# Kernel tuning notes

Measured on AMD Instinct MI355X. Metric: run time of the kernel, lower is better.

Reference implementation:

```python
import jax, jax.numpy as jnp
import numpy as np

B, N, M, K = 128, 128, 16, 8      # graphs, nodes/graph, num_samples, pearl_k
H_MLP = 16                        # pearl_mlp_out
D_PE = 64                         # pe_dims (GIN hidden/out)
E = 262144
BN_EPS = 1e-5


def setup_inputs() -> dict:
    key = jax.random.key(0)
    ks = jax.random.split(key, 16)
    lap = jax.random.normal(ks[0], (B, N, N), dtype=jnp.float32) * 0.1
    W0 = jax.random.normal(ks[1], (B, N, M), dtype=jnp.float32)
    edge_index = jax.random.randint(ks[2], (2, E), 0, B * N, dtype=jnp.int32)
    s = lambda k, sh, fan: jax.random.normal(k, sh, dtype=jnp.float32) / np.sqrt(fan)
    return {
        "lap": lap,
        "W0": W0,
        "mlp_W": s(ks[3], (K, H_MLP), K),
        "mlp_b": jnp.zeros((H_MLP,), jnp.float32),
        "bn_g": jnp.ones((H_MLP,), jnp.float32),
        "bn_b": jnp.zeros((H_MLP,), jnp.float32),
        "eps1": jnp.zeros((), jnp.float32),
        "W1a": s(ks[4], (H_MLP, D_PE), H_MLP),
        "b1a": jnp.zeros((D_PE,), jnp.float32),
        "W1b": s(ks[5], (D_PE, D_PE), D_PE),
        "b1b": jnp.zeros((D_PE,), jnp.float32),
        "eps2": jnp.zeros((), jnp.float32),
        "W2a": s(ks[6], (D_PE, D_PE), D_PE),
        "b2a": jnp.zeros((D_PE,), jnp.float32),
        "W2b": s(ks[7], (D_PE, D_PE), D_PE),
        "b2b": jnp.zeros((D_PE,), jnp.float32),
        "edge_index": edge_index,
    }


def _gin_layer(h, eps, Wa, ba, Wb, bb, src, dst, num_nodes):
    # h: [Nsum, M, D]; GIN aggregation: (1+eps)*h + sum_{j in N(i)} h_j
    agg = jax.ops.segment_sum(h[src], dst, num_segments=num_nodes)
    z = (1.0 + eps) * h + agg
    z = jax.nn.relu(jnp.einsum("nmd,de->nme", z, Wa) + ba)
    z = jnp.einsum("nmd,de->nme", z, Wb) + bb
    return jax.nn.relu(z)


def reference(lap, W0, mlp_W, mlp_b, bn_g, bn_b, eps1, W1a, b1a, W1b, b1b,
              eps2, W2a, b2a, W2b, b2b, edge_index):
    # polynomial filter: stack [W, S@W, S^2@W, ...]  -> [B, N, M, K]
    out = W0
    ws = [out]
    for _ in range(K - 1):
        out = jnp.einsum("bij,bjm->bim", lap, out)
        ws.append(out)
    feat = jnp.stack(ws, axis=-1)                       # [B, N, M, K]

    # per-graph MLP over trailing k dim + BatchNorm1d (training stats, per graph)
    h = jnp.einsum("bnmk,kh->bnmh", feat, mlp_W) + mlp_b  # [B, N, M, H]
    mu = jnp.mean(h, axis=(1, 2), keepdims=True)
    var = jnp.var(h, axis=(1, 2), keepdims=True)
    h = (h - mu) * jax.lax.rsqrt(var + BN_EPS) * bn_g + bn_b
    h = jax.nn.relu(h)

    # concat graphs -> [Nsum, M, H]; GIN over batched edge_index
    h = h.reshape(B * N, M, H_MLP)
    src, dst = edge_index[0], edge_index[1]
    h = _gin_layer(h, eps1, W1a, b1a, W1b, b1b, src, dst, B * N)
    h = _gin_layer(h, eps2, W2a, b2a, W2b, b2b, src, dst, B * N)

    # RandomSampleAggregator: sum over the sample dim -> [Nsum, D_pe]
    return h.sum(axis=1)
```

## Files before the change

### kernel.cpp

```cpp
#include <hip/hip_runtime.h>

typedef unsigned short u16;
typedef unsigned int   u32;
typedef short bf16x8 __attribute__((ext_vector_type(8)));
typedef float f32x4  __attribute__((ext_vector_type(4)));
typedef float f32x2  __attribute__((ext_vector_type(2)));

#define BG    128
#define NN    128
#define MS    16
#define KP    8
#define HM    16
#define DP    64
#define NSUM  16384
#define NE    262144
#define SITES 2048


__device__ __forceinline__ float blo(u32 u){ union{u32 i; float f;} v; v.i=u<<16; return v.f; }
__device__ __forceinline__ float bhi(u32 u){ union{u32 i; float f;} v; v.i=u&0xffff0000u; return v.f; }
__device__ __forceinline__ u16  f2b(float f){ union{float f; u32 i;} v; v.f=f; u32 x=v.i; x += 0x7fffu + ((x>>16)&1u); return (u16)(x>>16); }
__device__ __forceinline__ u32  pk2(float a, float b){ return (u32)f2b(a) | ((u32)f2b(b)<<16); }
__device__ __forceinline__ f32x2 up2(u32 u){ f32x2 v; v.x=blo(u); v.y=bhi(u); return v; }

__device__ __forceinline__ void fsplit(float x, short& hi, short& lo){
  u16 h = f2b(x); hi = (short)h; lo = (short)f2b(x - blo((u32)h));
}

#define MFMA16(a,b,c) __builtin_amdgcn_mfma_f32_16x16x32_bf16(a,b,c,0,0,0)

__device__ __forceinline__ bf16x8 bfragW(const float* __restrict__ W, int nrows,
                                         int k0, int nb, int col, int quad){
  bf16x8 f;
  #pragma unroll
  for(int j=0;j<8;++j){
    int k = k0 + quad*8 + j;
    float v = (k < nrows) ? W[k*DP + nb + col] : 0.f;
    f[j] = (short)f2b(v);
  }
  return f;
}
__device__ __forceinline__ bf16x8 afragT(const float* tp){
  float4 v0 = *(const float4*)tp;
  float4 v1 = *(const float4*)(tp+4);
  bf16x8 a;
  a[0]=(short)f2b(v0.x); a[1]=(short)f2b(v0.y); a[2]=(short)f2b(v0.z); a[3]=(short)f2b(v0.w);
  a[4]=(short)f2b(v1.x); a[5]=(short)f2b(v1.y); a[6]=(short)f2b(v1.z); a[7]=(short)f2b(v1.w);
  return a;
}

__global__ __launch_bounds__(256,1) void k_poly(
    const float* __restrict__ lap, const float* __restrict__ W0, const float* __restrict__ mlpW,
    const float* __restrict__ bng, const float* __restrict__ bnb, u16* __restrict__ h1T,
    int* __restrict__ cnt)
{
  __shared__ float Wbuf[2][SITES];
  __shared__ float mlpWS[KP*HM];
  __shared__ float red[4][32];
  __shared__ float stat[32];
  __shared__ float ssc[HM], ssh[HM];

  const int b = blockIdx.x, t = threadIdx.x, l = t&63, w = t>>6;
  const int col = l&15, quad = l>>4;
  if (t < 128) cnt[b*128 + t] = 0;

  {
    const float4* src = (const float4*)(W0 + (size_t)b*SITES);
    for (int i=t; i<SITES/4; i+=256) ((float4*)Wbuf[0])[i] = src[i];
    if (t < KP*HM) mlpWS[t] = mlpW[t];
  }

  bf16x8 Ah[2][4], Al[2][4];
  {
    const float* lg = lap + (size_t)b*NN*NN;
    #pragma unroll
    for(int Mt=0;Mt<2;++Mt){
      const int nr = w*32 + Mt*16 + col;
      #pragma unroll
      for(int Kc=0;Kc<4;++Kc){
        const float* p = lg + (size_t)nr*NN + Kc*32 + quad*8;
        float4 v0 = *(const float4*)p;
        float4 v1 = *(const float4*)(p+4);
        float xs[8] = {v0.x,v0.y,v0.z,v0.w,v1.x,v1.y,v1.z,v1.w};
        #pragma unroll
        for(int j=0;j<8;++j){ short hi,lo; fsplit(xs[j],hi,lo); Ah[Mt][Kc][j]=hi; Al[Mt][Kc][j]=lo; }
      }
    }
  }

  float h[8][16];
  {
    const float* w0g = W0 + (size_t)b*SITES;
    #pragma unroll
    for(int Mt=0;Mt<2;++Mt){
      #pragma unroll
      for(int r=0;r<4;++r){
        const int n = w*32 + Mt*16 + quad*4 + r;
        float sv = w0g[n*MS + col];
        #pragma unroll
        for(int c=0;c<16;++c) h[Mt*4+r][c] = sv*mlpW[c];
      }
    }
  }
  __syncthreads();

  int cur=0;
  for(int k=1;k<KP;++k){
    f32x4 c0 = {0.f,0.f,0.f,0.f};
    f32x4 c1 = {0.f,0.f,0.f,0.f};
    #pragma unroll
    for(int Kc=0;Kc<4;++Kc){
      const float* wb = &Wbuf[cur][(Kc*32 + quad*8)*MS + col];
      bf16x8 Bh, Bl;
      #pragma unroll
      for(int j=0;j<8;++j){
        float x = wb[j*MS];
        short hi,lo; fsplit(x,hi,lo); Bh[j]=hi; Bl[j]=lo;
      }
      c0 = MFMA16(Ah[0][Kc], Bh, c0);
      c0 = MFMA16(Ah[0][Kc], Bl, c0);
      c0 = MFMA16(Al[0][Kc], Bh, c0);
      c1 = MFMA16(Ah[1][Kc], Bh, c1);
      c1 = MFMA16(Ah[1][Kc], Bl, c1);
      c1 = MFMA16(Al[1][Kc], Bh, c1);
    }
    float mw[16];
    #pragma unroll
    for(int c=0;c<16;++c) mw[c]=mlpWS[k*16+c];
    #pragma unroll
    for(int r=0;r<4;++r){
      const int n0 = w*32 + quad*4 + r;
      Wbuf[cur^1][n0*MS + col]        = c0[r];
      Wbuf[cur^1][(n0+16)*MS + col]   = c1[r];
      #pragma unroll
      for(int c=0;c<16;++c){ h[r][c] += c0[r]*mw[c]; h[4+r][c] += c1[r]*mw[c]; }
    }
    __syncthreads();
    cur ^= 1;
  }

  float sum[16], sq[16];
  #pragma unroll
  for(int c=0;c<16;++c){ sum[c]=0.f; sq[c]=0.f; }
  #pragma unroll
  for(int s=0;s<8;++s){
    #pragma unroll
    for(int c=0;c<16;++c){ float v=h[s][c]; sum[c]+=v; sq[c]+=v*v; }
  }
  #pragma unroll
  for(int d=1;d<64;d<<=1){
    #pragma unroll
    for(int c=0;c<16;++c){ sum[c]+=__shfl_xor(sum[c],d,64); sq[c]+=__shfl_xor(sq[c],d,64); }
  }
  if(l==0){
    #pragma unroll
    for(int c=0;c<16;++c){ red[w][c]=sum[c]; red[w][16+c]=sq[c]; }
  }
  __syncthreads();
  if(t<32) stat[t]=red[0][t]+red[1][t]+red[2][t]+red[3][t];
  __syncthreads();
  if(t<16){
    float mu  = stat[t]*(1.f/SITES);
    float var = stat[16+t]*(1.f/SITES) - mu*mu;
    float sc  = bng[t] * rsqrtf(var + 1e-5f);
    ssc[t]=sc; ssh[t]=bnb[t] - mu*sc;
  }
  __syncthreads();
  {
    float sc[16], sh[16];
    #pragma unroll
    for(int c=0;c<16;++c){ sc[c]=ssc[c]; sh[c]=ssh[c]; }
    #pragma unroll
    for(int s=0;s<8;++s){
      const int n = w*32 + (s>>2)*16 + quad*4 + (s&3);
      const int node = b*NN + n;
      float r[16];
      #pragma unroll
      for(int c=0;c<16;++c) r[c]=fmaxf(h[s][c]*sc[c]+sh[c], 0.f);
      uint4 A;
      A.x=pk2(r[0],r[1]);  A.y=pk2(r[2],r[3]);  A.z=pk2(r[4],r[5]);  A.w=pk2(r[6],r[7]);
      uint4 Bv;
      Bv.x=pk2(r[8],r[9]); Bv.y=pk2(r[10],r[11]); Bv.z=pk2(r[12],r[13]); Bv.w=pk2(r[14],r[15]);
      u16* o = h1T + ((size_t)col*NSUM + node)*HM;
      *(uint4*)o     = A;
      *(uint4*)(o+8) = Bv;
    }
  }
}

__global__ void k_hist(const int* __restrict__ dst, int* __restrict__ cnt){
  int e = blockIdx.x*256 + threadIdx.x;
  atomicAdd(&cnt[dst[e]], 1);
}

__global__ void k_scan(const int* __restrict__ cnt, int* __restrict__ off, int* __restrict__ wpos){
  __shared__ int ps[256];
  const int t = threadIdx.x, PER = NSUM/256;
  int s=0;
  for(int i=0;i<PER;++i) s += cnt[t*PER+i];
  ps[t]=s; __syncthreads();
  for(int d=1; d<256; d<<=1){
    int v = (t>=d) ? ps[t-d] : 0;
    __syncthreads();
    ps[t] += v;
    __syncthreads();
  }
  int run = (t==0) ? 0 : ps[t-1];
  for(int i=0;i<PER;++i){
    int idx=t*PER+i;
    off[idx]=run; wpos[idx]=run;
    run += cnt[idx];
  }
  if(t==255) off[NSUM]=run;
}

__global__ void k_scatter(const int* __restrict__ srcI, const int* __restrict__ dstI,
                          int* __restrict__ wpos, int* __restrict__ srcs){
  int e = blockIdx.x*256 + threadIdx.x;
  int p = atomicAdd(&wpos[dstI[e]], 1);
  srcs[p] = srcI[e];
}

__global__ __launch_bounds__(256) void k_agg1(
  const u16* __restrict__ h1T, const float* __restrict__ eps1p,
  const int* __restrict__ off, const int* __restrict__ srcs, u16* __restrict__ z1)
{
  const int t=threadIdx.x, l=t&63, w=t>>6;
  const int m = blockIdx.x & 15, g = blockIdx.x >> 4;
  const int grp = l>>2, q = l&3;
  const int node = g*64 + w*16 + grp;
  const float epe = 1.f + eps1p[0];
  const u16* __restrict__ base = h1T + (size_t)m*NSUM*HM;

  f32x2 A[2];
  {
    uint2 x = *(const uint2*)&base[(size_t)node*HM + q*4];
    f32x2 s2; s2.x=epe; s2.y=epe;
    A[0]=s2*up2(x.x); A[1]=s2*up2(x.y);
  }
  const int e0 = off[node], e1 = off[node+1];
  int dmax = e1 - e0;
  #pragma unroll
  for(int d=1; d<64; d<<=1) dmax = max(dmax, __shfl_xor(dmax, d, 64));

  int i = 0;
  for(; i+2 <= dmax; i += 2){
    int pa = e0+i, pb = e0+i+1;
    float sa = (pa < e1) ? 1.f : 0.f;
    float sb = (pb < e1) ? 1.f : 0.f;
    int ea = min(pa, NE-1), eb = min(pb, NE-1);
    int ia = srcs[ea], ib = srcs[eb];
    uint2 xa = *(const uint2*)&base[(size_t)ia*HM + q*4];
    uint2 xb = *(const uint2*)&base[(size_t)ib*HM + q*4];
    f32x2 va; va.x=sa; va.y=sa;
    f32x2 vb; vb.x=sb; vb.y=sb;
    A[0]+=va*up2(xa.x); A[1]+=va*up2(xa.y);
    A[0]+=vb*up2(xb.x); A[1]+=vb*up2(xb.y);
  }
  if(i < dmax){
    int pa = e0+i;
    float sa = (pa < e1) ? 1.f : 0.f;
    int ea = min(pa, NE-1);
    int ia = srcs[ea];
    uint2 xa = *(const uint2*)&base[(size_t)ia*HM + q*4];
    f32x2 va; va.x=sa; va.y=sa;
    A[0]+=va*up2(xa.x); A[1]+=va*up2(xa.y);
  }

  uint2 o; o.x=pk2(A[0].x,A[0].y); o.y=pk2(A[1].x,A[1].y);
  *(uint2*)&z1[(size_t)node*256 + m*HM + q*4] = o;
}

__global__ __launch_bounds__(256) void k_agg2(
  const u16* __restrict__ h2T, const float* __restrict__ eps2p,
  const int* __restrict__ off, const int* __restrict__ srcs, u16* __restrict__ z2)
{
  const int t=threadIdx.x, l=t&63, w=t>>6;
  const int m = blockIdx.x & 15, g = blockIdx.x >> 4;
  const int grp = l>>3, q = l&7;
  const int node = g*32 + w*8 + grp;
  const float epe = 1.f + eps2p[0];
  const u16* __restrict__ base = h2T + (size_t)m*NSUM*DP;

  f32x2 A[4];
  {
    uint4 x = *(const uint4*)&base[(size_t)node*DP + q*8];
    f32x2 s2; s2.x=epe; s2.y=epe;
    A[0]=s2*up2(x.x); A[1]=s2*up2(x.y); A[2]=s2*up2(x.z); A[3]=s2*up2(x.w);
  }
  const int e0 = off[node], e1 = off[node+1];
  int dmax = e1 - e0;
  #pragma unroll
  for(int d=1; d<64; d<<=1) dmax = max(dmax, __shfl_xor(dmax, d, 64));

  int i = 0;
  for(; i+2 <= dmax; i += 2){
    int pa = e0+i, pb = e0+i+1;
    float sa = (pa < e1) ? 1.f : 0.f;
    float sb = (pb < e1) ? 1.f : 0.f;
    int ea = min(pa, NE-1), eb = min(pb, NE-1);
    int ia = srcs[ea], ib = srcs[eb];
    uint4 xa = *(const uint4*)&base[(size_t)ia*DP + q*8];
    uint4 xb = *(const uint4*)&base[(size_t)ib*DP + q*8];
    f32x2 va; va.x=sa; va.y=sa;
    f32x2 vb; vb.x=sb; vb.y=sb;
    A[0]+=va*up2(xa.x); A[1]+=va*up2(xa.y); A[2]+=va*up2(xa.z); A[3]+=va*up2(xa.w);
    A[0]+=vb*up2(xb.x); A[1]+=vb*up2(xb.y); A[2]+=vb*up2(xb.z); A[3]+=vb*up2(xb.w);
  }
  if(i < dmax){
    int pa = e0+i;
    float sa = (pa < e1) ? 1.f : 0.f;
    int ea = min(pa, NE-1);
    int ia = srcs[ea];
    uint4 xa = *(const uint4*)&base[(size_t)ia*DP + q*8];
    f32x2 va; va.x=sa; va.y=sa;
    A[0]+=va*up2(xa.x); A[1]+=va*up2(xa.y); A[2]+=va*up2(xa.z); A[3]+=va*up2(xa.w);
  }

  uint4 o;
  o.x=pk2(A[0].x,A[0].y); o.y=pk2(A[1].x,A[1].y);
  o.z=pk2(A[2].x,A[2].y); o.w=pk2(A[3].x,A[3].y);
  *(uint4*)&z2[(size_t)node*1024 + m*DP + q*8] = o;
}

__global__ __launch_bounds__(256) void k_mm1(
  const u16* __restrict__ z1, const float* __restrict__ W1a, const float* __restrict__ b1a,
  const float* __restrict__ W1b, const float* __restrict__ b1b, u16* __restrict__ h2T)
{
  __shared__ float tS[4][16*68 + 4];
  const int t=threadIdx.x, l=t&63, w=t>>6;
  const int col=l&15, quad=l>>4;

  bf16x8 fa[4], fb[4][2];
  float bav[4], bbv[4];
  #pragma unroll
  for(int nt=0;nt<4;++nt){
    fa[nt]    = bfragW(W1a, HM, 0,  nt*16, col, quad);
    fb[nt][0] = bfragW(W1b, DP, 0,  nt*16, col, quad);
    fb[nt][1] = bfragW(W1b, DP, 32, nt*16, col, quad);
    bav[nt] = b1a[nt*16+col];
    bbv[nt] = b1b[nt*16+col];
  }
  for(int ni=0;ni<2;++ni){
    const int node = blockIdx.x*8 + ni*4 + w;
    bf16x8 a0;
    #pragma unroll
    for(int j=0;j<8;++j) a0[j]=0;
    if (quad < 2) a0 = *(const bf16x8*)&z1[(size_t)node*256 + col*16 + quad*8];
    #pragma unroll
    for(int nt=0;nt<4;++nt){
      f32x4 c = {bav[nt], bav[nt], bav[nt], bav[nt]};
      c = MFMA16(a0, fa[nt], c);
      #pragma unroll
      for(int r=0;r<4;++r)
        tS[w][(quad*4+r)*68 + nt*16 + col] = fmaxf(c[r], 0.f);
    }
    bf16x8 ta0 = afragT(&tS[w][col*68 + quad*8]);
    bf16x8 ta1 = afragT(&tS[w][col*68 + 32 + quad*8]);
    #pragma unroll
    for(int nt=0;nt<4;++nt){
      f32x4 c = {bbv[nt], bbv[nt], bbv[nt], bbv[nt]};
      c = MFMA16(ta0, fb[nt][0], c);
      c = MFMA16(ta1, fb[nt][1], c);
      #pragma unroll
      for(int r=0;r<4;++r)
        h2T[((size_t)(quad*4+r)*NSUM + node)*DP + nt*16 + col] = f2b(fmaxf(c[r], 0.f));
    }
  }
}

__global__ __launch_bounds__(256) void k_mm2(
  const u16* __restrict__ z2, const float* __restrict__ W2a, const float* __restrict__ b2a,
  const float* __restrict__ W2b, const float* __restrict__ b2b, float* __restrict__ out)
{
  __shared__ float tS[4][16*68 + 4];
  const int t=threadIdx.x, l=t&63, w=t>>6;
  const int col=l&15, quad=l>>4;

  bf16x8 fa[4][2], fb[4][2];
  float bav[4], bbv[4];
  #pragma unroll
  for(int nt=0;nt<4;++nt){
    fa[nt][0] = bfragW(W2a, DP, 0,  nt*16, col, quad);
    fa[nt][1] = bfragW(W2a, DP, 32, nt*16, col, quad);
    fb[nt][0] = bfragW(W2b, DP, 0,  nt*16, col, quad);
    fb[nt][1] = bfragW(W2b, DP, 32, nt*16, col, quad);
    bav[nt] = b2a[nt*16+col];
    bbv[nt] = b2b[nt*16+col];
  }
  for(int ni=0;ni<2;++ni){
    const int node = blockIdx.x*8 + ni*4 + w;
    const u16* zrow = &z2[(size_t)node*1024];
    bf16x8 a0 = *(const bf16x8*)&zrow[col*64 + quad*8];
    bf16x8 a1 = *(const bf16x8*)&zrow[col*64 + quad*8 + 32];
    #pragma unroll
    for(int nt=0;nt<4;++nt){
      f32x4 c = {bav[nt], bav[nt], bav[nt], bav[nt]};
      c = MFMA16(a0, fa[nt][0], c);
      c = MFMA16(a1, fa[nt][1], c);
      #pragma unroll
      for(int r=0;r<4;++r)
        tS[w][(quad*4+r)*68 + nt*16 + col] = fmaxf(c[r], 0.f);
    }
    bf16x8 ta0 = afragT(&tS[w][col*68 + quad*8]);
    bf16x8 ta1 = afragT(&tS[w][col*68 + 32 + quad*8]);
    #pragma unroll
    for(int nt=0;nt<4;++nt){
      f32x4 c = {bbv[nt], bbv[nt], bbv[nt], bbv[nt]};
      c = MFMA16(ta0, fb[nt][0], c);
      c = MFMA16(ta1, fb[nt][1], c);
      float s = fmaxf(c[0],0.f)+fmaxf(c[1],0.f)+fmaxf(c[2],0.f)+fmaxf(c[3],0.f);
      s += __shfl_xor(s, 16, 64);
      s += __shfl_xor(s, 32, 64);
      if (quad == 0)
        out[(size_t)node*64 + nt*16 + col] = s;
    }
  }
}

extern "C" void kernel_launch(void* const* d_in, const int* in_sizes, int n_in,
                              void* d_out, int out_size, void* d_ws, size_t ws_size,
                              hipStream_t stream)
{
  (void)in_sizes; (void)n_in; (void)out_size; (void)ws_size;
  const float* lap  = (const float*)d_in[0];
  const float* W0   = (const float*)d_in[1];
  const float* mlpW = (const float*)d_in[2];
  const float* bng  = (const float*)d_in[4];
  const float* bnb  = (const float*)d_in[5];
  const float* eps1 = (const float*)d_in[6];
  const float* W1a  = (const float*)d_in[7];
  const float* b1a  = (const float*)d_in[8];
  const float* W1b  = (const float*)d_in[9];
  const float* b1b  = (const float*)d_in[10];
  const float* eps2 = (const float*)d_in[11];
  const float* W2a  = (const float*)d_in[12];
  const float* b2a  = (const float*)d_in[13];
  const float* W2b  = (const float*)d_in[14];
  const float* b2b  = (const float*)d_in[15];
  const int*   ei   = (const int*)d_in[16];
  const int* srcI = ei;
  const int* dstI = ei + NE;

  char* ws = (char*)d_ws;
  u16* h1T  = (u16*)(ws);
  u16* z1   = (u16*)(ws + 8388608);
  u16* h2T  = (u16*)(ws + 16777216);
  u16* z2   = (u16*)(ws + 50331648);
  int* cnt  = (int*)(ws + 83886080);
  int* offA = (int*)(ws + 83951616);
  int* wpos = (int*)(ws + 84017408);
  int* srcs = (int*)(ws + 84082944);

  k_poly   <<<BG,      256, 0, stream>>>(lap, W0, mlpW, bng, bnb, h1T, cnt);
  k_hist   <<<NE/256,  256, 0, stream>>>(dstI, cnt);
  k_scan   <<<1,       256, 0, stream>>>(cnt, offA, wpos);
  k_scatter<<<NE/256,  256, 0, stream>>>(srcI, dstI, wpos, srcs);
  k_agg1   <<<16*(NSUM/64), 256, 0, stream>>>(h1T, eps1, offA, srcs, z1);
  k_mm1    <<<NSUM/8,  256, 0, stream>>>(z1, W1a, b1a, W1b, b1b, h2T);
  k_agg2   <<<16*(NSUM/32), 256, 0, stream>>>(h2T, eps2, offA, srcs, z2);
  k_mm2    <<<NSUM/8,  256, 0, stream>>>(z2, W2a, b2a, W2b, b2b, (float*)d_out);
}
```

Before: 274.7 us.

## Sort nodes by in-degree to balance wave work in GIN aggregation

Adds a single-block counting sort that orders nodes by in-degree into a permutation array (reusing the wpos buffer). Both aggregation kernels now take node indices from this permutation, so each wavefront handles nodes of similar degree and wastes fewer iterations when looping up to the wave-wide maximum degree. k_agg1 also widens each lane to 8 features (uint4 loads/stores) with 2 lanes per node, doubling nodes per wave. The cost is an extra serial single-block kernel launch and scattered output writes.

```diff
diff --git a/kernel.cpp b/kernel.cpp
--- a/kernel.cpp
+++ b/kernel.cpp
@@ -221,22 +221,50 @@
   srcs[p] = srcI[e];
 }
 
+__global__ __launch_bounds__(256) void k_sort(const int* __restrict__ cnt, int* __restrict__ perm){
+  __shared__ int bins[256];
+  __shared__ int base[256];
+  const int t = threadIdx.x;
+  bins[t]=0;
+  __syncthreads();
+  for(int i=t;i<NSUM;i+=256){
+    int d = min(cnt[i],255);
+    atomicAdd(&bins[d],1);
+  }
+  __syncthreads();
+  int v = bins[t];
+  for(int d=1; d<256; d<<=1){
+    int u = (t>=d) ? bins[t-d] : 0;
+    __syncthreads();
+    bins[t] += u;
+    __syncthreads();
+  }
+  base[t] = bins[t] - v;
+  __syncthreads();
+  for(int i=t;i<NSUM;i+=256){
+    int d = min(cnt[i],255);
+    int p = atomicAdd(&base[d],1);
+    perm[p] = i;
+  }
+}
+
 __global__ __launch_bounds__(256) void k_agg1(
   const u16* __restrict__ h1T, const float* __restrict__ eps1p,
-  const int* __restrict__ off, const int* __restrict__ srcs, u16* __restrict__ z1)
+  const int* __restrict__ off, const int* __restrict__ srcs,
+  const int* __restrict__ perm, u16* __restrict__ z1)
 {
   const int t=threadIdx.x, l=t&63, w=t>>6;
   const int m = blockIdx.x & 15, g = blockIdx.x >> 4;
-  const int grp = l>>2, q = l&3;
-  const int node = g*64 + w*16 + grp;
+  const int grp = l>>1, q = l&1;
+  const int node = perm[g*128 + w*32 + grp];
   const float epe = 1.f + eps1p[0];
   const u16* __restrict__ base = h1T + (size_t)m*NSUM*HM;
 
-  f32x2 A[2];
-  {
-    uint2 x = *(const uint2*)&base[(size_t)node*HM + q*4];
+  f32x2 A[4];
+  {
+    uint4 x = *(const uint4*)&base[(size_t)node*HM + q*8];
     f32x2 s2; s2.x=epe; s2.y=epe;
-    A[0]=s2*up2(x.x); A[1]=s2*up2(x.y);
+    A[0]=s2*up2(x.x); A[1]=s2*up2(x.y); A[2]=s2*up2(x.z); A[3]=s2*up2(x.w);
   }
   const int e0 = off[node], e1 = off[node+1];
   int dmax = e1 - e0;
@@ -250,35 +278,38 @@
     float sb = (pb < e1) ? 1.f : 0.f;
     int ea = min(pa, NE-1), eb = min(pb, NE-1);
     int ia = srcs[ea], ib = srcs[eb];
-    uint2 xa = *(const uint2*)&base[(size_t)ia*HM + q*4];
-    uint2 xb = *(const uint2*)&base[(size_t)ib*HM + q*4];
+    uint4 xa = *(const uint4*)&base[(size_t)ia*HM + q*8];
+    uint4 xb = *(const uint4*)&base[(size_t)ib*HM + q*8];
     f32x2 va; va.x=sa; va.y=sa;
     f32x2 vb; vb.x=sb; vb.y=sb;
-    A[0]+=va*up2(xa.x); A[1]+=va*up2(xa.y);
-    A[0]+=vb*up2(xb.x); A[1]+=vb*up2(xb.y);
+    A[0]+=va*up2(xa.x); A[1]+=va*up2(xa.y); A[2]+=va*up2(xa.z); A[3]+=va*up2(xa.w);
+    A[0]+=vb*up2(xb.x); A[1]+=vb*up2(xb.y); A[2]+=vb*up2(xb.z); A[3]+=vb*up2(xb.w);
   }
   if(i < dmax){
     int pa = e0+i;
     float sa = (pa < e1) ? 1.f : 0.f;
     int ea = min(pa, NE-1);
     int ia = srcs[ea];
-    uint2 xa = *(const uint2*)&base[(size_t)ia*HM + q*4];
+    uint4 xa = *(const uint4*)&base[(size_t)ia*HM + q*8];
     f32x2 va; va.x=sa; va.y=sa;
-    A[0]+=va*up2(xa.x); A[1]+=va*up2(xa.y);
-  }
-
-  uint2 o; o.x=pk2(A[0].x,A[0].y); o.y=pk2(A[1].x,A[1].y);
-  *(uint2*)&z1[(size_t)node*256 + m*HM + q*4] = o;
+    A[0]+=va*up2(xa.x); A[1]+=va*up2(xa.y); A[2]+=va*up2(xa.z); A[3]+=va*up2(xa.w);
+  }
+
+  uint4 o;
+  o.x=pk2(A[0].x,A[0].y); o.y=pk2(A[1].x,A[1].y);
+  o.z=pk2(A[2].x,A[2].y); o.w=pk2(A[3].x,A[3].y);
+  *(uint4*)&z1[(size_t)node*256 + m*HM + q*8] = o;
 }
 
 __global__ __launch_bounds__(256) void k_agg2(
   const u16* __restrict__ h2T, const float* __restrict__ eps2p,
-  const int* __restrict__ off, const int* __restrict__ srcs, u16* __restrict__ z2)
+  const int* __restrict__ off, const int* __restrict__ srcs,
+  const int* __restrict__ perm, u16* __restrict__ z2)
 {
   const int t=threadIdx.x, l=t&63, w=t>>6;
   const int m = blockIdx.x & 15, g = blockIdx.x >> 4;
   const int grp = l>>3, q = l&7;
-  const int node = g*32 + w*8 + grp;
+  const int node = perm[g*32 + w*8 + grp];
   const float epe = 1.f + eps2p[0];
   const u16* __restrict__ base = h2T + (size_t)m*NSUM*DP;
 
@@ -451,13 +482,15 @@
   int* offA = (int*)(ws + 83951616);
   int* wpos = (int*)(ws + 84017408);
   int* srcs = (int*)(ws + 84082944);
+  int* perm = wpos;
 
   k_poly   <<<BG,      256, 0, stream>>>(lap, W0, mlpW, bng, bnb, h1T, cnt);
   k_hist   <<<NE/256,  256, 0, stream>>>(dstI, cnt);
   k_scan   <<<1,       256, 0, stream>>>(cnt, offA, wpos);
   k_scatter<<<NE/256,  256, 0, stream>>>(srcI, dstI, wpos, srcs);
-  k_agg1   <<<16*(NSUM/64), 256, 0, stream>>>(h1T, eps1, offA, srcs, z1);
+  k_sort   <<<1,       256, 0, stream>>>(cnt, perm);
+  k_agg1   <<<16*(NSUM/128), 256, 0, stream>>>(h1T, eps1, offA, srcs, perm, z1);
   k_mm1    <<<NSUM/8,  256, 0, stream>>>(z1, W1a, b1a, W1b, b1b, h2T);
-  k_agg2   <<<16*(NSUM/32), 256, 0, stream>>>(h2T, eps2, offA, srcs, z2);
+  k_agg2   <<<16*(NSUM/32), 256, 0, stream>>>(h2T, eps2, offA, srcs, perm, z2);
   k_mm2    <<<NSUM/8,  256, 0, stream>>>(z2, W2a, b2a, W2b, b2b, (float*)d_out);
 }
```

After: 289.4 us. 1.05x slower.
